# Kernel tuning notes

Hardware: AMD Instinct MI355X
Metric: run time of the kernel (lower is better)

## Reference

```python
import jax, jax.numpy as jnp
import numpy as np

NUM_GROUPS = 32
EPS = 1e-5  # torch GroupNorm default


def group_norm(x, gamma, beta):
    # x: [B, C, T, H, W]; normalize each (b, t) frame per channel-group (CausalNormalize)
    B, C, T, H, W = x.shape
    xg = x.reshape(B, NUM_GROUPS, C // NUM_GROUPS, T, H, W)
    mu = xg.mean(axis=(2, 4, 5), keepdims=True)
    var = xg.var(axis=(2, 4, 5), keepdims=True)
    xn = ((xg - mu) * jax.lax.rsqrt(var + EPS)).reshape(B, C, T, H, W)
    return xn * gamma[None, :, None, None, None] + beta[None, :, None, None, None]


def setup_inputs() -> dict:
    key = jax.random.key(0)
    ks = jax.random.split(key, 8)
    B, C, T, H, W = 2, 512, 16, 32, 32
    S, D = 64, 1024  # context_T = 4 * T, context_dim
    wscale = 0.02
    return {
        "x": jax.random.normal(ks[0], (B, C, T, H, W), jnp.float32),
        "context": jax.random.normal(ks[1], (B, S, D), jnp.float32),
        "gamma": jnp.ones((C,), jnp.float32),
        "beta": jnp.zeros((C,), jnp.float32),
        "wq": jax.random.normal(ks[2], (C, C), jnp.float32) * wscale,
        "bq": jnp.zeros((C,), jnp.float32),
        "wkv": jax.random.normal(ks[3], (2 * C, D), jnp.float32) * wscale,
        "bkv": jnp.zeros((2 * C,), jnp.float32),
        "wo": jax.random.normal(ks[4], (C, C), jnp.float32) * wscale,
        "bo": jnp.zeros((C,), jnp.float32),
    }


def reference(x, context, gamma, beta, wq, bq, wkv, bkv, wo, bo):
    B, C, T, H, W = x.shape
    S = context.shape[1]
    n = S // T  # context frames per x frame (assert S % T == 0 in original)

    h = group_norm(x, gamma, beta)
    # q_proj: CausalConv3d with kernel 1, padding 0 == pointwise channel linear
    q = jnp.einsum('bcthw,oc->bothw', h, wq) + bq[None, :, None, None, None]

    kv = jnp.einsum('bsd,od->bso', context, wkv) + bkv  # [B, S, 2C]
    k, v = jnp.split(kv, 2, axis=-1)                    # each [B, S, C]

    # space2batch: [B,C,T,H,W] -> [B, H*W, T, C] (batch-major, queries per spatial pos)
    qb = q.transpose(0, 3, 4, 2, 1).reshape(B, H * W, T, C)

    # attention; kv broadcast over H*W done implicitly via einsum
    scores = jnp.einsum('bptc,bsc->bpts', qb, k) * (C ** -0.5)
    # block-causal mask: row i attends to context positions < (i+1)*n
    mask = jnp.arange(S)[None, :] < jnp.minimum((jnp.arange(T) + 1) * n, S)[:, None]
    scores = jnp.where(mask[None, None], scores, -jnp.inf)
    w = jax.nn.softmax(scores, axis=-1)
    o = jnp.einsum('bpts,bsc->bptc', w, v)              # [B, HW, T, C]

    # batch2space: back to [B, C, T, H, W]
    o = o.reshape(B, H, W, T, C).transpose(0, 4, 3, 1, 2)
    o = jnp.einsum('bcthw,oc->bothw', o, wo) + bo[None, :, None, None, None]
    return x + o
```

## Files before the change

kernel.cpp:

```cpp
#include <hip/hip_runtime.h>


typedef float    f32x4 __attribute__((ext_vector_type(4)));
typedef _Float16 half8 __attribute__((ext_vector_type(8)));
typedef _Float16 half4 __attribute__((ext_vector_type(4)));

#define GLB_AS __attribute__((address_space(1)))
#define LDS_AS __attribute__((address_space(3)))

__device__ __forceinline__ void gload_lds16(const void* g, void* l) {
  __builtin_amdgcn_global_load_lds((const GLB_AS void*)g, (LDS_AS void*)l, 16, 0, 0);
}

__global__ __launch_bounds__(256) void gn_fused(const float* __restrict__ x,
                                                const float* __restrict__ gamma,
                                                const float* __restrict__ beta,
                                                _Float16* __restrict__ h)
{
  const int t = blockIdx.x, g = blockIdx.y, b = blockIdx.z;
  const int tid = threadIdx.x;
  __shared__ float tile[16 * 1028];
  __shared__ float red[2][4];
  const long xbase = ((long)((b * 512 + g * 16) * 16 + t)) << 10;

  float s1 = 0.f, s2 = 0.f;
#pragma unroll
  for (int i = 0; i < 16; ++i) {
    const int idx = i * 256 + tid;
    const int c = idx >> 8;
    const int p = (idx & 255) * 4;
    const f32x4 v = *(const f32x4*)&x[xbase + ((long)c << 14) + p];
    s1 += v[0] + v[1] + v[2] + v[3];
    s2 += v[0] * v[0] + v[1] * v[1] + v[2] * v[2] + v[3] * v[3];
    *(f32x4*)&tile[c * 1028 + p] = v;
  }
  for (int o = 32; o; o >>= 1) { s1 += __shfl_down(s1, o); s2 += __shfl_down(s2, o); }
  if ((tid & 63) == 0) { red[0][tid >> 6] = s1; red[1][tid >> 6] = s2; }
  __syncthreads();
  const float a  = red[0][0] + red[0][1] + red[0][2] + red[0][3];
  const float qq = red[1][0] + red[1][1] + red[1][2] + red[1][3];
  const float mu = a * (1.f / 16384.f);
  const float rs = rsqrtf(qq * (1.f / 16384.f) - mu * mu + 1e-5f);

  float scv[16], ocv[16];
#pragma unroll
  for (int c4 = 0; c4 < 4; ++c4) {
    const f32x4 gv = *(const f32x4*)&gamma[g * 16 + c4 * 4];
    const f32x4 bv = *(const f32x4*)&beta[g * 16 + c4 * 4];
#pragma unroll
    for (int j = 0; j < 4; ++j) {
      scv[c4 * 4 + j] = rs * gv[j];
      ocv[c4 * 4 + j] = bv[j] - mu * scv[c4 * 4 + j];
    }
  }

  const long hbase = (((long)b * 16384 + (long)t * 1024) << 9) + g * 16;
#pragma unroll
  for (int it = 0; it < 4; ++it) {
    const int p = it * 256 + tid;
    half8 h0, h1;
#pragma unroll
    for (int c = 0; c < 16; ++c) {
      const _Float16 hv = (_Float16)(tile[c * 1028 + p] * scv[c] + ocv[c]);
      if (c < 8) h0[c] = hv; else h1[c - 8] = hv;
    }
    *(half8*)&h[hbase + (long)p * 512]     = h0;
    *(half8*)&h[hbase + (long)p * 512 + 8] = h1;
  }
}

__global__ void to_f16(const float* __restrict__ src, _Float16* __restrict__ dst, int n4)
{
  const int i = blockIdx.x * blockDim.x + threadIdx.x;
  if (i >= n4) return;
  const f32x4 v = *(const f32x4*)&src[i * 4];
  half4 hh;
#pragma unroll
  for (int j = 0; j < 4; ++j) hh[j] = (_Float16)v[j];
  *(half4*)&dst[i * 4] = hh;
}

__global__ __launch_bounds__(256) void kv_gemm(const float* __restrict__ ctx,
                                               const float* __restrict__ wkv,
                                               const float* __restrict__ bkv,
                                               _Float16* __restrict__ kOut,
                                               _Float16* __restrict__ vT)
{
  const int b = blockIdx.y;
  const int o0 = blockIdx.x * 16;
  const int tid = threadIdx.x, l = tid & 63, w = tid >> 6;
  __shared__ float cbuf[64 * 64];
  __shared__ float wbuf[16 * 64];
  float acc[4] = {0.f, 0.f, 0.f, 0.f};

  for (int dc = 0; dc < 16; ++dc) {
#pragma unroll
    for (int i = 0; i < 4; ++i) {
      const int lin = tid + i * 256;
      const int s = lin >> 4, c4 = lin & 15;
      *(f32x4*)&cbuf[s * 64 + ((c4 ^ (s & 15)) << 2)] =
          *(const f32x4*)&ctx[((long)(b * 64 + s) << 10) + dc * 64 + c4 * 4];
    }
    {
      const int o = tid >> 4, c4 = tid & 15;
      *(f32x4*)&wbuf[o * 64 + c4 * 4] =
          *(const f32x4*)&wkv[((long)(o0 + o) << 10) + dc * 64 + c4 * 4];
    }
    __syncthreads();
#pragma unroll
    for (int d4 = 0; d4 < 16; ++d4) {
      const f32x4 cv = *(const f32x4*)&cbuf[l * 64 + ((d4 ^ (l & 15)) << 2)];
#pragma unroll
      for (int j = 0; j < 4; ++j) {
        const f32x4 wv = *(const f32x4*)&wbuf[(w * 4 + j) * 64 + (d4 << 2)];
        acc[j] += cv[0] * wv[0] + cv[1] * wv[1] + cv[2] * wv[2] + cv[3] * wv[3];
      }
    }
    __syncthreads();
  }
#pragma unroll
  for (int j = 0; j < 4; ++j) {
    const int o = o0 + w * 4 + j;
    const float r = acc[j] + bkv[o];
    if (o < 512) kOut[((long)(b * 64 + l) << 9) + o] = (_Float16)r;
    else         vT[((long)(b * 512 + (o - 512)) << 6) + l] = (_Float16)r;
  }
}

#define BM 128
#define BN 128
#define BK 32

template <int BIAS_PER_N, int RESID, int OUT16, int SWZ>
__global__ __launch_bounds__(256) void gemm_f16(
    const _Float16* __restrict__ A, const _Float16* __restrict__ B,
    void* __restrict__ Cv, const float* __restrict__ bias, const float* __restrict__ resid,
    int K, int lda, int ldb, int ldc,
    long aBatch, long bBatch, long cBatch, long rBatch)
{
  __shared__ _Float16 sA[2][BM * BK];
  __shared__ _Float16 sB[2][BN * BK];
  const int tid = threadIdx.x;
  const int lane = tid & 63;
  const int w = tid >> 6;
  const int bz = blockIdx.z;

  int bx, by;
  if (SWZ == 1) {
    const int f = blockIdx.x;
    const int nf = ((f & 7) << 6) | (f >> 3);
    bx = nf & 3; by = nf >> 2;
  } else if (SWZ == 2) {
    const int f = blockIdx.x;
    const int nf = ((f & 7) << 6) | (f >> 3);
    bx = nf >> 2; by = nf & 3;
  } else {
    bx = blockIdx.x; by = blockIdx.y;
  }

  const long m0 = (long)bx * BM;
  const long n0 = (long)by * BN;
  const _Float16* pA = A + bz * aBatch + m0 * lda;
  const _Float16* pB = B + bz * bBatch + n0 * ldb;
  const int srow = lane & 15;
  const int schunk = (lane >> 4) * 8;
  const int wm = w >> 1, wn = w & 1;

  f32x4 acc[4][4] = {};

  auto stage = [&](int buf, int k0) {
#pragma unroll
    for (int i = 0; i < 2; ++i) {
      const int r = w * 32 + i * 16 + srow;
      const int lbase = (w * 32 + i * 16) * BK;
      gload_lds16(pA + (long)r * lda + k0 + schunk, &sA[buf][lbase]);
      gload_lds16(pB + (long)r * ldb + k0 + schunk, &sB[buf][lbase]);
    }
  };

  stage(0, 0);
  __syncthreads();
  int cur = 0;
  for (int k0 = 0; k0 < K; k0 += BK) {
    if (k0 + BK < K) stage(cur ^ 1, k0 + BK);
    half8 ah[4], bh[4];
#pragma unroll
    for (int mi = 0; mi < 4; ++mi)
      ah[mi] = *(const half8*)&sA[cur][(wm * 4 + mi) * 512 + lane * 8];
#pragma unroll
    for (int ni = 0; ni < 4; ++ni)
      bh[ni] = *(const half8*)&sB[cur][(wn * 4 + ni) * 512 + lane * 8];
#pragma unroll
    for (int mi = 0; mi < 4; ++mi)
#pragma unroll
      for (int ni = 0; ni < 4; ++ni)
        acc[mi][ni] = __builtin_amdgcn_mfma_f32_16x16x32_f16(ah[mi], bh[ni], acc[mi][ni], 0, 0, 0);
    __syncthreads();
    cur ^= 1;
  }

  const long cb = bz * cBatch;
  const long rb = bz * rBatch;
#pragma unroll
  for (int mi = 0; mi < 4; ++mi) {
#pragma unroll
    for (int ni = 0; ni < 4; ++ni) {
      const long row = m0 + wm * 64 + mi * 16 + (lane >> 4) * 4;
      const long col = n0 + wn * 64 + ni * 16 + (lane & 15);
#pragma unroll
      for (int j = 0; j < 4; ++j) {
        float v = acc[mi][ni][j];
        v += BIAS_PER_N ? bias[col] : bias[row + j];
        if (RESID) v += resid[rb + (row + j) * ldc + col];
        if (OUT16) ((_Float16*)Cv)[cb + (row + j) * ldc + col] = (_Float16)v;
        else       ((float*)Cv)[cb + (row + j) * ldc + col] = v;
      }
    }
  }
}

__global__ __launch_bounds__(256) void attn2(const _Float16* __restrict__ q,
                                             const _Float16* __restrict__ k,
                                             const _Float16* __restrict__ vT,
                                             _Float16* __restrict__ O)
{
  const int tid = threadIdx.x;
  const int l = tid & 63, w = tid >> 6;
  const int b = blockIdx.z, t = blockIdx.y;
  const int p0 = t * 1024 + blockIdx.x * 64 + w * 16;
  const int lim = (t + 1) * 4;
  const int nf = (t >> 2) + 1;
  const int ks = (t >> 3) + 1;
  const int cl = l & 15;
  const int g8 = (l >> 4) * 8;
  const int r4 = (l >> 4) * 4;

  __shared__ _Float16 wlds[4][16][72];

  f32x4 sc[4] = {};
  const _Float16* qb = q + (((long)(b * 16384 + p0 + cl)) << 9) + g8;
  const _Float16* kb = k + (((long)(b * 64 + cl)) << 9) + g8;
#pragma unroll
  for (int kk = 0; kk < 16; ++kk) {
    const half8 af = *(const half8*)(qb + kk * 32);
#pragma unroll
    for (int f = 0; f < 4; ++f)
      if (f < nf)
        sc[f] = __builtin_amdgcn_mfma_f32_16x16x32_f16(
            af, *(const half8*)(kb + f * (16 * 512) + kk * 32), sc[f], 0, 0, 0);
  }

  const float SCALE = 0.044194173824159216f;
  float ex[4][4], mj[4], sj[4];
#pragma unroll
  for (int j = 0; j < 4; ++j) {
    float mx = -1e30f;
#pragma unroll
    for (int f = 0; f < 4; ++f) {
      float v = sc[f][j] * SCALE;
      if (f * 16 + cl >= lim) v = -1e30f;
      ex[f][j] = v;
      mx = fmaxf(mx, v);
    }
    mj[j] = mx;
  }
#pragma unroll
  for (int o = 1; o < 16; o <<= 1)
#pragma unroll
    for (int j = 0; j < 4; ++j) mj[j] = fmaxf(mj[j], __shfl_xor(mj[j], o));
#pragma unroll
  for (int j = 0; j < 4; ++j) {
    float s = 0.f;
#pragma unroll
    for (int f = 0; f < 4; ++f) {
      const float e = __expf(ex[f][j] - mj[j]);
      ex[f][j] = e;
      s += e;
    }
    sj[j] = s;
  }
#pragma unroll
  for (int o = 1; o < 16; o <<= 1)
#pragma unroll
    for (int j = 0; j < 4; ++j) sj[j] += __shfl_xor(sj[j], o);
#pragma unroll
  for (int j = 0; j < 4; ++j) {
    const float inv = 1.f / sj[j];
#pragma unroll
    for (int f = 0; f < 4; ++f)
      wlds[w][r4 + j][f * 16 + cl] = (_Float16)(ex[f][j] * inv);
  }

  const half8 wa0 = *(const half8*)&wlds[w][cl][g8];
  const half8 wa1 = *(const half8*)&wlds[w][cl][32 + g8];
#pragma unroll
  for (int hf = 0; hf < 2; ++hf) {
    f32x4 oc[16] = {};
#pragma unroll
    for (int cf = 0; cf < 16; ++cf) {
      const _Float16* vb = vT + (((long)(b * 512 + hf * 256 + cf * 16 + cl)) << 6) + g8;
      oc[cf] = __builtin_amdgcn_mfma_f32_16x16x32_f16(wa0, *(const half8*)vb, oc[cf], 0, 0, 0);
      if (ks == 2)
        oc[cf] = __builtin_amdgcn_mfma_f32_16x16x32_f16(wa1, *(const half8*)(vb + 32), oc[cf], 0, 0, 0);
    }
#pragma unroll
    for (int cf = 0; cf < 16; ++cf)
#pragma unroll
      for (int j = 0; j < 4; ++j)
        O[(((long)(b * 16384 + p0 + r4 + j)) << 9) + hf * 256 + cf * 16 + cl] =
            (_Float16)oc[cf][j];
  }
}

extern "C" void kernel_launch(void* const* d_in, const int* in_sizes, int n_in,
                              void* d_out, int out_size, void* d_ws, size_t ws_size,
                              hipStream_t stream)
{
  (void)in_sizes; (void)n_in; (void)out_size; (void)ws_size;
  const float* x     = (const float*)d_in[0];
  const float* ctx   = (const float*)d_in[1];
  const float* gamma = (const float*)d_in[2];
  const float* beta  = (const float*)d_in[3];
  const float* wq    = (const float*)d_in[4];
  const float* bq    = (const float*)d_in[5];
  const float* wkv   = (const float*)d_in[6];
  const float* bkv   = (const float*)d_in[7];
  const float* wo    = (const float*)d_in[8];
  const float* bo    = (const float*)d_in[9];
  float* out = (float*)d_out;

  char* ws = (char*)d_ws;
  size_t off = 0;
  auto alloc = [&](size_t bytes) -> void* {
    void* p = ws + off;
    off += (bytes + 255) & ~(size_t)255;
    return p;
  };
  const long HPC = 8388608;
  _Float16* hF   = (_Float16*)alloc(2 * HPC * 2);
  _Float16* qF   = (_Float16*)alloc(2 * HPC * 2);
  _Float16* wqF  = (_Float16*)alloc(512 * 512 * 2);
  _Float16* woF  = (_Float16*)alloc(512 * 512 * 2);
  _Float16* kF   = (_Float16*)alloc(2 * 64 * 512 * 2);
  _Float16* vTF  = (_Float16*)alloc(2 * 512 * 64 * 2);
  _Float16* oF   = hF;

  gn_fused<<<dim3(16, 32, 2), 256, 0, stream>>>(x, gamma, beta, hF);
  to_f16<<<dim3(256), 256, 0, stream>>>(wq, wqF, 65536);
  to_f16<<<dim3(256), 256, 0, stream>>>(wo, woF, 65536);
  kv_gemm<<<dim3(64, 2), 256, 0, stream>>>(ctx, wkv, bkv, kF, vTF);

  gemm_f16<1, 0, 1, 2><<<dim3(512, 1, 2), 256, 0, stream>>>(
      hF, wqF, qF, bq, nullptr, 512, 512, 512, 512, HPC, 0, HPC, 0);

  attn2<<<dim3(16, 16, 2), 256, 0, stream>>>(qF, kF, vTF, oF);

  gemm_f16<0, 1, 0, 1><<<dim3(512, 1, 2), 256, 0, stream>>>(
      woF, oF, out, bo, x, 512, 512, 512, 16384, 0, HPC, HPC, HPC);
}
```

Before: 306.6 us.

## Fuse Q projection, attention, and output projection into one kernel

Replaces the separate Q-projection GEMM, attention kernel, and output-projection GEMM with a single kernel that handles 128 spatial positions per block. Q and the attention output stay in LDS (swizzled) instead of making a full fp16 round-trip through global memory, and two launches are removed. In exchange each block is large, using about 88KB of LDS and many accumulators. Only 256 blocks are launched, so occupancy and parallelism drop, and wq and wo are read directly from global memory with no LDS staging.

```diff
diff --git a/kernel.cpp b/kernel.cpp
--- a/kernel.cpp
+++ b/kernel.cpp
@@ -127,188 +127,210 @@
   }
 }
 
-#define BM 128
-#define BN 128
-#define BK 32
-
-template <int BIAS_PER_N, int RESID, int OUT16, int SWZ>
-__global__ __launch_bounds__(256) void gemm_f16(
-    const _Float16* __restrict__ A, const _Float16* __restrict__ B,
-    void* __restrict__ Cv, const float* __restrict__ bias, const float* __restrict__ resid,
-    int K, int lda, int ldb, int ldc,
-    long aBatch, long bBatch, long cBatch, long rBatch)
-{
-  __shared__ _Float16 sA[2][BM * BK];
-  __shared__ _Float16 sB[2][BN * BK];
-  const int tid = threadIdx.x;
-  const int lane = tid & 63;
-  const int w = tid >> 6;
-  const int bz = blockIdx.z;
-
-  int bx, by;
-  if (SWZ == 1) {
-    const int f = blockIdx.x;
-    const int nf = ((f & 7) << 6) | (f >> 3);
-    bx = nf & 3; by = nf >> 2;
-  } else if (SWZ == 2) {
-    const int f = blockIdx.x;
-    const int nf = ((f & 7) << 6) | (f >> 3);
-    bx = nf >> 2; by = nf & 3;
-  } else {
-    bx = blockIdx.x; by = blockIdx.y;
-  }
-
-  const long m0 = (long)bx * BM;
-  const long n0 = (long)by * BN;
-  const _Float16* pA = A + bz * aBatch + m0 * lda;
-  const _Float16* pB = B + bz * bBatch + n0 * ldb;
-  const int srow = lane & 15;
-  const int schunk = (lane >> 4) * 8;
-  const int wm = w >> 1, wn = w & 1;
-
-  f32x4 acc[4][4] = {};
-
-  auto stage = [&](int buf, int k0) {
-#pragma unroll
-    for (int i = 0; i < 2; ++i) {
-      const int r = w * 32 + i * 16 + srow;
-      const int lbase = (w * 32 + i * 16) * BK;
-      gload_lds16(pA + (long)r * lda + k0 + schunk, &sA[buf][lbase]);
-      gload_lds16(pB + (long)r * ldb + k0 + schunk, &sB[buf][lbase]);
-    }
-  };
-
-  stage(0, 0);
-  __syncthreads();
-  int cur = 0;
-  for (int k0 = 0; k0 < K; k0 += BK) {
-    if (k0 + BK < K) stage(cur ^ 1, k0 + BK);
-    half8 ah[4], bh[4];
-#pragma unroll
-    for (int mi = 0; mi < 4; ++mi)
-      ah[mi] = *(const half8*)&sA[cur][(wm * 4 + mi) * 512 + lane * 8];
-#pragma unroll
-    for (int ni = 0; ni < 4; ++ni)
-      bh[ni] = *(const half8*)&sB[cur][(wn * 4 + ni) * 512 + lane * 8];
-#pragma unroll
-    for (int mi = 0; mi < 4; ++mi)
-#pragma unroll
-      for (int ni = 0; ni < 4; ++ni)
-        acc[mi][ni] = __builtin_amdgcn_mfma_f32_16x16x32_f16(ah[mi], bh[ni], acc[mi][ni], 0, 0, 0);
-    __syncthreads();
-    cur ^= 1;
-  }
-
-  const long cb = bz * cBatch;
-  const long rb = bz * rBatch;
-#pragma unroll
-  for (int mi = 0; mi < 4; ++mi) {
-#pragma unroll
-    for (int ni = 0; ni < 4; ++ni) {
-      const long row = m0 + wm * 64 + mi * 16 + (lane >> 4) * 4;
-      const long col = n0 + wn * 64 + ni * 16 + (lane & 15);
-#pragma unroll
-      for (int j = 0; j < 4; ++j) {
-        float v = acc[mi][ni][j];
-        v += BIAS_PER_N ? bias[col] : bias[row + j];
-        if (RESID) v += resid[rb + (row + j) * ldc + col];
-        if (OUT16) ((_Float16*)Cv)[cb + (row + j) * ldc + col] = (_Float16)v;
-        else       ((float*)Cv)[cb + (row + j) * ldc + col] = v;
-      }
-    }
-  }
-}
-
-__global__ __launch_bounds__(256) void attn2(const _Float16* __restrict__ q,
-                                             const _Float16* __restrict__ k,
-                                             const _Float16* __restrict__ vT,
-                                             _Float16* __restrict__ O)
+__global__ __launch_bounds__(512) void fused_qao(
+    const _Float16* __restrict__ h,
+    const _Float16* __restrict__ wq,
+    const float* __restrict__ bq,
+    const _Float16* __restrict__ kM,
+    const _Float16* __restrict__ vT,
+    const _Float16* __restrict__ wo,
+    const float* __restrict__ bo,
+    const float* __restrict__ xr,
+    float* __restrict__ out)
 {
   const int tid = threadIdx.x;
   const int l = tid & 63, w = tid >> 6;
-  const int b = blockIdx.z, t = blockIdx.y;
-  const int p0 = t * 1024 + blockIdx.x * 64 + w * 16;
+  const int b = blockIdx.y;
+  const int p0 = blockIdx.x * 128;
+  const int t = p0 >> 10;
   const int lim = (t + 1) * 4;
-  const int nf = (t >> 2) + 1;
-  const int ks = (t >> 3) + 1;
-  const int cl = l & 15;
-  const int g8 = (l >> 4) * 8;
-  const int r4 = (l >> 4) * 4;
-
-  __shared__ _Float16 wlds[4][16][72];
-
-  f32x4 sc[4] = {};
-  const _Float16* qb = q + (((long)(b * 16384 + p0 + cl)) << 9) + g8;
-  const _Float16* kb = k + (((long)(b * 64 + cl)) << 9) + g8;
-#pragma unroll
-  for (int kk = 0; kk < 16; ++kk) {
-    const half8 af = *(const half8*)(qb + kk * 32);
-#pragma unroll
-    for (int f = 0; f < 4; ++f)
-      if (f < nf)
-        sc[f] = __builtin_amdgcn_mfma_f32_16x16x32_f16(
-            af, *(const half8*)(kb + f * (16 * 512) + kk * 32), sc[f], 0, 0, 0);
-  }
-
-  const float SCALE = 0.044194173824159216f;
-  float ex[4][4], mj[4], sj[4];
-#pragma unroll
-  for (int j = 0; j < 4; ++j) {
-    float mx = -1e30f;
-#pragma unroll
-    for (int f = 0; f < 4; ++f) {
-      float v = sc[f][j] * SCALE;
-      if (f * 16 + cl >= lim) v = -1e30f;
-      ex[f][j] = v;
-      mx = fmaxf(mx, v);
-    }
-    mj[j] = mx;
-  }
-#pragma unroll
-  for (int o = 1; o < 16; o <<= 1)
-#pragma unroll
-    for (int j = 0; j < 4; ++j) mj[j] = fmaxf(mj[j], __shfl_xor(mj[j], o));
-#pragma unroll
-  for (int j = 0; j < 4; ++j) {
-    float s = 0.f;
-#pragma unroll
-    for (int f = 0; f < 4; ++f) {
-      const float e = __expf(ex[f][j] - mj[j]);
-      ex[f][j] = e;
-      s += e;
-    }
-    sj[j] = s;
-  }
-#pragma unroll
-  for (int o = 1; o < 16; o <<= 1)
-#pragma unroll
-    for (int j = 0; j < 4; ++j) sj[j] += __shfl_xor(sj[j], o);
-#pragma unroll
-  for (int j = 0; j < 4; ++j) {
-    const float inv = 1.f / sj[j];
-#pragma unroll
-    for (int f = 0; f < 4; ++f)
-      wlds[w][r4 + j][f * 16 + cl] = (_Float16)(ex[f][j] * inv);
-  }
-
-  const half8 wa0 = *(const half8*)&wlds[w][cl][g8];
-  const half8 wa1 = *(const half8*)&wlds[w][cl][32 + g8];
-#pragma unroll
-  for (int hf = 0; hf < 2; ++hf) {
-    f32x4 oc[16] = {};
-#pragma unroll
-    for (int cf = 0; cf < 16; ++cf) {
-      const _Float16* vb = vT + (((long)(b * 512 + hf * 256 + cf * 16 + cl)) << 6) + g8;
-      oc[cf] = __builtin_amdgcn_mfma_f32_16x16x32_f16(wa0, *(const half8*)vb, oc[cf], 0, 0, 0);
-      if (ks == 2)
-        oc[cf] = __builtin_amdgcn_mfma_f32_16x16x32_f16(wa1, *(const half8*)(vb + 32), oc[cf], 0, 0, 0);
-    }
-#pragma unroll
-    for (int cf = 0; cf < 16; ++cf)
-#pragma unroll
-      for (int j = 0; j < 4; ++j)
-        O[(((long)(b * 16384 + p0 + r4 + j)) << 9) + hf * 256 + cf * 16 + cl] =
-            (_Float16)oc[cf][j];
+  const int nfc = (t >> 2) + 1;
+  const int ksc = (t >> 3) + 1;
+  const int cl = l & 15, kc = l >> 4, r4 = (l >> 4) * 4;
+
+  __shared__ _Float16 qbuf[128 * 256];
+  __shared__ _Float16 hstage[2][128 * 32];
+  __shared__ _Float16 pbuf[128 * 64];
+
+  const int swA = (cl >> 1) & 3;
+  const int sw7 = cl & 7;
+  const int wm2 = w >> 2, wn4 = w & 3;
+  const int wm4 = w >> 1, wn2 = w & 1;
+
+  const int srow = 16 * w + (l >> 2);
+  const int schunk = (l & 3) ^ ((l >> 3) & 3);
+  const _Float16* hsrc = h + (((long)(b * 16384 + p0 + srow)) << 9) + schunk * 8;
+  _Float16* hdst0 = &hstage[0][w * 512];
+  _Float16* hdst1 = &hstage[1][w * 512];
+
+  f32x4 acc_s[4] = {};
+
+  for (int ch = 0; ch < 2; ++ch) {
+    f32x4 accq[4][4] = {};
+    gload_lds16(hsrc, hdst0);
+    __syncthreads();
+    int cur = 0;
+    for (int ks = 0; ks < 16; ++ks) {
+      const int k0 = ks * 32;
+      if (ks < 15) gload_lds16(hsrc + k0 + 32, cur ? hdst0 : hdst1);
+      half8 ah[4], bh[4];
+#pragma unroll
+      for (int ni = 0; ni < 4; ++ni)
+        bh[ni] = *(const half8*)&wq[((long)(ch * 256 + wn4 * 64 + ni * 16 + cl) << 9) + k0 + kc * 8];
+#pragma unroll
+      for (int mi = 0; mi < 4; ++mi)
+        ah[mi] = *(const half8*)&hstage[cur][(wm2 * 64 + mi * 16 + cl) * 32 + ((kc ^ swA) * 8)];
+#pragma unroll
+      for (int mi = 0; mi < 4; ++mi)
+#pragma unroll
+        for (int ni = 0; ni < 4; ++ni)
+          accq[mi][ni] = __builtin_amdgcn_mfma_f32_16x16x32_f16(ah[mi], bh[ni], accq[mi][ni], 0, 0, 0);
+      __syncthreads();
+      cur ^= 1;
+    }
+#pragma unroll
+    for (int mi = 0; mi < 4; ++mi) {
+#pragma unroll
+      for (int ni = 0; ni < 4; ++ni) {
+        const int col = wn4 * 64 + ni * 16 + cl;
+        const float bqv = bq[ch * 256 + col];
+#pragma unroll
+        for (int j = 0; j < 4; ++j) {
+          const int row = wm2 * 64 + mi * 16 + r4 + j;
+          qbuf[row * 256 + (((col >> 3) ^ (row & 7)) * 8) + (col & 7)] =
+              (_Float16)(accq[mi][ni][j] + bqv);
+        }
+      }
+    }
+    __syncthreads();
+    {
+      const int qrow = 16 * w + cl;
+#pragma unroll
+      for (int ks = 0; ks < 8; ++ks) {
+        const half8 af = *(const half8*)&qbuf[qrow * 256 + (((ks * 4 + kc) ^ sw7) * 8)];
+#pragma unroll
+        for (int ni = 0; ni < 4; ++ni)
+          if (ni < nfc)
+            acc_s[ni] = __builtin_amdgcn_mfma_f32_16x16x32_f16(
+                af,
+                *(const half8*)&kM[((long)(b * 64 + ni * 16 + cl) << 9) + ch * 256 + ks * 32 + kc * 8],
+                acc_s[ni], 0, 0, 0);
+      }
+    }
+    __syncthreads();
+  }
+
+  {
+    const float SCALE = 0.044194173824159216f;
+    float ex[4][4], mj[4], sj[4];
+#pragma unroll
+    for (int j = 0; j < 4; ++j) {
+      float mx = -1e30f;
+#pragma unroll
+      for (int ni = 0; ni < 4; ++ni) {
+        const float v = (ni * 16 + cl < lim) ? acc_s[ni][j] * SCALE : -1e30f;
+        ex[ni][j] = v;
+        mx = fmaxf(mx, v);
+      }
+      mj[j] = mx;
+    }
+#pragma unroll
+    for (int o = 1; o < 16; o <<= 1)
+#pragma unroll
+      for (int j = 0; j < 4; ++j) mj[j] = fmaxf(mj[j], __shfl_xor(mj[j], o));
+#pragma unroll
+    for (int j = 0; j < 4; ++j) {
+      float s = 0.f;
+#pragma unroll
+      for (int ni = 0; ni < 4; ++ni) {
+        const float e = __expf(ex[ni][j] - mj[j]);
+        ex[ni][j] = e;
+        s += e;
+      }
+      sj[j] = s;
+    }
+#pragma unroll
+    for (int o = 1; o < 16; o <<= 1)
+#pragma unroll
+      for (int j = 0; j < 4; ++j) sj[j] += __shfl_xor(sj[j], o);
+#pragma unroll
+    for (int j = 0; j < 4; ++j) {
+      const float inv = 1.f / sj[j];
+      const int row = 16 * w + r4 + j;
+#pragma unroll
+      for (int ni = 0; ni < 4; ++ni) {
+        const int col = ni * 16 + cl;
+        pbuf[row * 64 + (((col >> 3) ^ (row & 7)) * 8) + (col & 7)] =
+            (_Float16)(ex[ni][j] * inv);
+      }
+    }
+  }
+  __syncthreads();
+
+  f32x4 acc_out[8][4] = {};
+  for (int ch = 0; ch < 2; ++ch) {
+    f32x4 acco[4][4] = {};
+#pragma unroll
+    for (int ks = 0; ks < 2; ++ks) {
+      if (ks < ksc) {
+        half8 af[4];
+#pragma unroll
+        for (int mi = 0; mi < 4; ++mi)
+          af[mi] = *(const half8*)&pbuf[(wm2 * 64 + mi * 16 + cl) * 64 + (((ks * 4 + kc) ^ sw7) * 8)];
+#pragma unroll
+        for (int mi = 0; mi < 4; ++mi)
+#pragma unroll
+          for (int ni = 0; ni < 4; ++ni)
+            acco[mi][ni] = __builtin_amdgcn_mfma_f32_16x16x32_f16(
+                af[mi],
+                *(const half8*)&vT[((long)(b * 512 + ch * 256 + wn4 * 64 + ni * 16 + cl) << 6) + ks * 32 + kc * 8],
+                acco[mi][ni], 0, 0, 0);
+      }
+    }
+#pragma unroll
+    for (int mi = 0; mi < 4; ++mi) {
+#pragma unroll
+      for (int ni = 0; ni < 4; ++ni) {
+        const int col = wn4 * 64 + ni * 16 + cl;
+#pragma unroll
+        for (int j = 0; j < 4; ++j) {
+          const int row = wm2 * 64 + mi * 16 + r4 + j;
+          qbuf[row * 256 + (((col >> 3) ^ (row & 7)) * 8) + (col & 7)] = (_Float16)acco[mi][ni][j];
+        }
+      }
+    }
+    __syncthreads();
+#pragma unroll
+    for (int ks = 0; ks < 8; ++ks) {
+      half8 aw[8], bh[4];
+#pragma unroll
+      for (int mi = 0; mi < 8; ++mi)
+        aw[mi] = *(const half8*)&wo[((long)(wm4 * 128 + mi * 16 + cl) << 9) + ch * 256 + ks * 32 + kc * 8];
+#pragma unroll
+      for (int ni = 0; ni < 4; ++ni)
+        bh[ni] = *(const half8*)&qbuf[(wn2 * 64 + ni * 16 + cl) * 256 + (((ks * 4 + kc) ^ sw7) * 8)];
+#pragma unroll
+      for (int mi = 0; mi < 8; ++mi)
+#pragma unroll
+        for (int ni = 0; ni < 4; ++ni)
+          acc_out[mi][ni] = __builtin_amdgcn_mfma_f32_16x16x32_f16(aw[mi], bh[ni], acc_out[mi][ni], 0, 0, 0);
+    }
+    __syncthreads();
+  }
+
+#pragma unroll
+  for (int mi = 0; mi < 8; ++mi) {
+#pragma unroll
+    for (int j = 0; j < 4; ++j) {
+      const int o = wm4 * 128 + mi * 16 + r4 + j;
+      const float bov = bo[o];
+      const long obase = (long)b * 8388608 + ((long)o << 14) + p0;
+#pragma unroll
+      for (int ni = 0; ni < 4; ++ni) {
+        const int p = wn2 * 64 + ni * 16 + cl;
+        out[obase + p] = acc_out[mi][ni][j] + bov + xr[obase + p];
+      }
+    }
   }
 }
 
@@ -338,23 +360,16 @@
   };
   const long HPC = 8388608;
   _Float16* hF   = (_Float16*)alloc(2 * HPC * 2);
-  _Float16* qF   = (_Float16*)alloc(2 * HPC * 2);
   _Float16* wqF  = (_Float16*)alloc(512 * 512 * 2);
   _Float16* woF  = (_Float16*)alloc(512 * 512 * 2);
   _Float16* kF   = (_Float16*)alloc(2 * 64 * 512 * 2);
   _Float16* vTF  = (_Float16*)alloc(2 * 512 * 64 * 2);
-  _Float16* oF   = hF;
 
   gn_fused<<<dim3(16, 32, 2), 256, 0, stream>>>(x, gamma, beta, hF);
   to_f16<<<dim3(256), 256, 0, stream>>>(wq, wqF, 65536);
   to_f16<<<dim3(256), 256, 0, stream>>>(wo, woF, 65536);
   kv_gemm<<<dim3(64, 2), 256, 0, stream>>>(ctx, wkv, bkv, kF, vTF);
 
-  gemm_f16<1, 0, 1, 2><<<dim3(512, 1, 2), 256, 0, stream>>>(
-      hF, wqF, qF, bq, nullptr, 512, 512, 512, 512, HPC, 0, HPC, 0);
-
-  attn2<<<dim3(16, 16, 2), 256, 0, stream>>>(qF, kF, vTF, oF);
-
-  gemm_f16<0, 1, 0, 1><<<dim3(512, 1, 2), 256, 0, stream>>>(
-      woF, oF, out, bo, x, 512, 512, 512, 16384, 0, HPC, HPC, HPC);
-}
+  fused_qao<<<dim3(128, 2), 512, 0, stream>>>(
+      hF, wqF, bq, kF, vTF, woF, bo, x, out);
+}
```

Result: no change. 306.4 us (-0.1%).
